# Performance work log

Hardware: AMD Instinct MI355X
Metric: run time of the kernel (lower is better)

## Reference

```python
import jax, jax.numpy as jnp
import numpy as np

N = 8192
TOKEN_DIM = 384
K = 16
D_IN = 2 * (TOKEN_DIM + 3)  # 774


def setup_inputs() -> dict:
    key = jax.random.key(0)
    k1, k2, k3, k4, k5, k6 = jax.random.split(key, 6)
    xyz = jax.random.normal(k1, (N, 3), dtype=jnp.float32)
    feat = jax.random.normal(k2, (N, TOKEN_DIM), dtype=jnp.float32)
    W1 = jax.random.normal(k3, (D_IN, TOKEN_DIM), dtype=jnp.float32) / np.sqrt(D_IN)
    b1 = jax.random.normal(k4, (TOKEN_DIM,), dtype=jnp.float32) * 0.01
    W2 = jax.random.normal(k5, (TOKEN_DIM, 3), dtype=jnp.float32) / np.sqrt(TOKEN_DIM)
    b2 = jax.random.normal(k6, (3,), dtype=jnp.float32) * 0.01
    return {"xyz": xyz, "feat": feat, "W1": W1, "b1": b1, "W2": W2, "b2": b2}


def _knn_idx(xyz, k):
    # pairwise squared distances [N, N]; loop=False -> exclude self via +inf diag
    sq = jnp.sum(xyz * xyz, axis=-1)
    d2 = sq[:, None] + sq[None, :] - 2.0 * (xyz @ xyz.T)
    n = xyz.shape[0]
    d2 = jnp.where(jnp.eye(n, dtype=bool), jnp.inf, d2)
    _, idx = jax.lax.top_k(-d2, k)  # idx[i] = k nearest neighbors (sources) of target i
    return idx


def reference(xyz, feat, W1, b1, W2, b2):
    idx = _knn_idx(xyz, K)                      # [N, K] int32
    x = jnp.concatenate([feat, xyz], axis=-1)   # [N, D] with D = token_dim + 3
    x_j = x[idx]                                # [N, K, D] gathered neighbor feats
    x_i = x[:, None, :]                         # [N, 1, D]
    # EdgeConv message: nn(cat([x_i, x_j - x_i]))
    e = jnp.concatenate([jnp.broadcast_to(x_i, x_j.shape), x_j - x_i], axis=-1)  # [N, K, 2D]
    h = jax.nn.relu(jnp.einsum('nkd,df->nkf', e, W1) + b1)   # [N, K, token_dim]
    m = jnp.einsum('nkf,fo->nko', h, W2) + b2                # [N, K, 3]
    agg = jnp.max(m, axis=1)                                 # max aggregation over neighbors
    return xyz + agg
```

## Files before the change

kernel.cpp:

```cpp
#include <hip/hip_runtime.h>
#include <hip/hip_bf16.h>


#define N 8192
#define TD 384
#define KNN 16
#define DX 387
#define KP 416
#define NF 768
#define INFF __builtin_inff()

typedef __attribute__((ext_vector_type(8))) short short8;
typedef __attribute__((ext_vector_type(4))) float f32x4;
typedef __attribute__((ext_vector_type(2))) float f32x2;


__device__ __forceinline__ f32x2 pk_mul(f32x2 a, f32x2 b) {
    f32x2 r; asm("v_pk_mul_f32 %0, %1, %2" : "=v"(r) : "v"(a), "v"(b)); return r;
}
__device__ __forceinline__ f32x2 pk_add(f32x2 a, f32x2 b) {
    f32x2 r; asm("v_pk_add_f32 %0, %1, %2" : "=v"(r) : "v"(a), "v"(b)); return r;
}
__device__ __forceinline__ f32x2 pk_sub(f32x2 a, f32x2 b) {
    f32x2 r; asm("v_pk_add_f32 %0, %1, %2 neg_lo:[0,1] neg_hi:[0,1]" : "=v"(r) : "v"(a), "v"(b)); return r;
}
__device__ __forceinline__ f32x2 pk_fma(f32x2 a, f32x2 b, f32x2 c) {
    f32x2 r; asm("v_pk_fma_f32 %0, %1, %2, %3" : "=v"(r) : "v"(a), "v"(b), "v"(c)); return r;
}

__device__ __forceinline__ void dist4(f32x2 qx, f32x2 qy, f32x2 qz, f32x2 qw,
                                      f32x2 x01, f32x2 x23, f32x2 y01, f32x2 y23,
                                      f32x2 z01, f32x2 z23, f32x2 s01, f32x2 s23,
                                      f32x2& d01, f32x2& d23) {
    f32x2 dot01 = pk_fma(qz, z01, pk_fma(qy, y01, pk_mul(qx, x01)));
    f32x2 dot23 = pk_fma(qz, z23, pk_fma(qy, y23, pk_mul(qx, x23)));
    d01 = pk_sub(pk_add(qw, s01), pk_add(dot01, dot01));
    d23 = pk_sub(pk_add(qw, s23), pk_add(dot23, dot23));
}

__device__ __forceinline__ int xbin(float x) {
    int b = (int)((x + 4.0f) * 32.0f);
    return b < 0 ? 0 : (b > 255 ? 255 : b);
}


__global__ void __launch_bounds__(128) prep_all(const float* __restrict__ feat,
                                                const float* __restrict__ xyz,
                                                const float* __restrict__ W1,
                                                __hip_bfloat16* __restrict__ Xb,
                                                __hip_bfloat16* __restrict__ Wpt,
                                                int* __restrict__ cut) {
    int b = blockIdx.x;
    int t = threadIdx.x;
    if (b < N) {
        if (t < 96) {
            float4 f = reinterpret_cast<const float4*>(feat + (size_t)b*TD)[t];
            __hip_bfloat16 h[4] = {__float2bfloat16(f.x), __float2bfloat16(f.y),
                                   __float2bfloat16(f.z), __float2bfloat16(f.w)};
            *reinterpret_cast<ulonglong1*>(Xb + b*KP + t*4) = *reinterpret_cast<ulonglong1*>(h);
        } else {
            int d = TD + (t - 96);
            float v = (d < DX) ? xyz[b*3 + (d - TD)] : 0.f;
            Xb[b*KP + d] = __float2bfloat16(v);
        }
    } else if (b < N + NF) {
        int f = b - N;
        for (int k = t; k < KP; k += 128) {
            float v = 0.f;
            if (k < DX) {
                if (f < TD) v = W1[k*TD + f] - W1[(DX+k)*TD + f];
                else        v = W1[(DX+k)*TD + (f - TD)];
            }
            Wpt[f*KP + k] = __float2bfloat16(v);
        }
    } else {
        cut[t] = 0;
        cut[t + 128] = 0;
    }
}


__global__ void __launch_bounds__(256) assign_kernel(const float* __restrict__ xyz,
                                                     int* __restrict__ cut,
                                                     int* __restrict__ tlo,
                                                     int* __restrict__ thi,
                                                     float* __restrict__ stile) {
    __shared__ int hcnt[256];
    __shared__ int base[256];
    __shared__ int stlo[32], sthi[32];
    const int t = threadIdx.x;

    hcnt[t] = 0;
    if (t < 32) { stlo[t] = 255; sthi[t] = 0; }
    __syncthreads();

    #pragma unroll
    for (int c = 0; c < 32; ++c) {
        atomicAdd(&hcnt[xbin(xyz[(t + c*256)*3])], 1);
    }
    __syncthreads();

    const int v = hcnt[t];
    base[t] = v;
    __syncthreads();
    for (int off = 1; off < 256; off <<= 1) {
        int add = (t >= off) ? base[t - off] : 0;
        __syncthreads();
        base[t] += add;
        __syncthreads();
    }
    const int end = base[t], start = end - v;
    __syncthreads();
    base[t] = start;
    __syncthreads();

    if (blockIdx.x == 0) {
        if (v > 0) {
            for (int x = start >> 8; x <= (end - 1) >> 8; ++x) {
                atomicMin(&stlo[x], t);
                atomicMax(&sthi[x], t);
            }
        }
        __syncthreads();
        if (t < 32) { tlo[t] = stlo[t]; thi[t] = sthi[t]; }
    }

    const int i = blockIdx.x * 256 + t;
    float x = xyz[i*3+0], y = xyz[i*3+1], z = xyz[i*3+2];
    int bin = xbin(x);
    int pos = base[bin] + atomicAdd(&cut[bin], 1);
    float sq = __fadd_rn(__fadd_rn(__fmul_rn(x,x), __fmul_rn(y,y)), __fmul_rn(z,z));
    float* tp = stile + (pos >> 8) * 1280 + (pos & 255);
    tp[0] = x; tp[256] = y; tp[512] = z; tp[768] = sq;
    reinterpret_cast<int*>(tp)[1024] = i;
}


__device__ __forceinline__ float rdlane_f(float v, int src) {
    return __uint_as_float(__builtin_amdgcn_readlane(__float_as_uint(v), src));
}
__device__ __forceinline__ unsigned udmap(float x) {
    unsigned u = __float_as_uint(x);
    return ((int)u < 0) ? ~u : (u | 0x80000000u);
}


__global__ void __launch_bounds__(256, 6) knn_kernel(const float* __restrict__ stile,
                                                     const int* __restrict__ tlo,
                                                     const int* __restrict__ thi,
                                                     int* __restrict__ knn) {
    __shared__ float    dcache[4][5][256];
    __shared__ unsigned sbuf[4][128][2];
    const int lane = threadIdx.x & 63;
    const int wv   = threadIdx.x >> 6;
    const int s    = blockIdx.x * 4 + wv;
    const int tq   = s >> 8;
    const int sl   = (s & 255) >> 2;
    const int slot = s & 3;

    const float* qp = stile + tq*1280 + (s & 255);
    const float qx = qp[0], qy = qp[256], qz = qp[512], qw = qp[768];
    const int   qi = reinterpret_cast<const int*>(qp)[1024];
    const f32x2 qx2 = {qx,qx}, qy2 = {qy,qy}, qz2 = {qz,qz}, qw2 = {qw,qw};

    const float* lbase = stile + lane*4;
    const bool is_self_lane = (lane == sl);

    float mn = INFF;
    int lo = tq - 2; if (lo < 0) lo = 0; if (lo > 27) lo = 27;
    #pragma unroll
    for (int tt = 0; tt < 5; ++tt) {
        const int t = lo + tt;
        const float* tp = lbase + t*1280;
        float4 X = *(const float4*)(tp);
        float4 Y = *(const float4*)(tp + 256);
        float4 Z = *(const float4*)(tp + 512);
        float4 S = *(const float4*)(tp + 768);
        f32x2 x01 = {X.x,X.y}, x23 = {X.z,X.w};
        f32x2 y01 = {Y.x,Y.y}, y23 = {Y.z,Y.w};
        f32x2 z01 = {Z.x,Z.y}, z23 = {Z.z,Z.w};
        f32x2 s01 = {S.x,S.y}, s23 = {S.z,S.w};
        f32x2 d01, d23;
        dist4(qx2, qy2, qz2, qw2, x01, x23, y01, y23, z01, z23, s01, s23, d01, d23);
        if ((t == tq) && is_self_lane) {
            if      (slot == 0) d01[0] = INFF;
            else if (slot == 1) d01[1] = INFF;
            else if (slot == 2) d23[0] = INFF;
            else                d23[1] = INFF;
        }
        f32x4 dd = {d01[0], d01[1], d23[0], d23[1]};
        *reinterpret_cast<f32x4*>(&dcache[wv][tt][lane*4]) = dd;
        mn = fminf(mn, fminf(fminf(dd[0], dd[1]), fminf(dd[2], dd[3])));
    }

    float T;
    {
        unsigned ub = udmap(mn);
        unsigned long long alive = ~0ull;
        int need = KNN;
        #pragma unroll
        for (int b = 31; b >= 0; --b) {
            unsigned long long ones  = __ballot(((ub >> b) & 1u) != 0u);
            unsigned long long zeros = alive & ~ones;
            int cz = (int)__popcll(zeros);
            bool tz = (cz >= need);
            alive = tz ? zeros : (alive & ones);
            need  = tz ? need : (need - cz);
        }
        T = fmaxf(rdlane_f(mn, (int)__ffsll(alive) - 1), 0.f);
    }

    unsigned mask;
    {
        const int ti = lane & 31;
        const int bl = tlo[ti], bh = thi[ti];
        const float xlo = (bl == 0)   ? -1e30f : (bl * 0.03125f - 4.0f);
        const float xhi = (bh == 255) ?  1e30f : ((bh + 1) * 0.03125f - 4.0f);
        float gap = fmaxf(0.f, fmaxf(xlo - qx, qx - xhi));
        bool gate = (gap * gap <= T + 1e-3f);
        mask = (unsigned)__ballot(gate && (lane < 32));
    }

    int cnt = 0;
    const unsigned long long ltm = (1ull << lane) - 1;

    auto push = [&](float dv, int idx) {
        bool pred = (dv <= T);
        unsigned long long bal = __ballot(pred);
        if (bal) {
            int posn = cnt + (int)__popcll(bal & ltm);
            if (pred && posn < 128) {
                sbuf[wv][posn][0] = udmap(dv);
                sbuf[wv][posn][1] = (unsigned)idx;
            }
            cnt += (int)__popcll(bal);
        }
    };

    #pragma unroll
    for (int tt = 0; tt < 5; ++tt) {
        const int t = lo + tt;
        if (!((mask >> t) & 1u)) continue;
        f32x4 dd = *reinterpret_cast<const f32x4*>(&dcache[wv][tt][lane*4]);
        int4 I = *(const int4*)(lbase + t*1280 + 1024);
        push(dd[0], I.x);
        push(dd[1], I.y);
        push(dd[2], I.z);
        push(dd[3], I.w);
    }
    unsigned rest = mask & ~(0x1Fu << lo);
    while (rest) {
        const int t = (int)__ffs(rest) - 1;
        rest &= rest - 1;
        const float* tp = lbase + t*1280;
        float4 X = *(const float4*)(tp);
        float4 Y = *(const float4*)(tp + 256);
        float4 Z = *(const float4*)(tp + 512);
        float4 S = *(const float4*)(tp + 768);
        int4   I = *(const int4*)(tp + 1024);
        f32x2 x01 = {X.x,X.y}, x23 = {X.z,X.w};
        f32x2 y01 = {Y.x,Y.y}, y23 = {Y.z,Y.w};
        f32x2 z01 = {Z.x,Z.y}, z23 = {Z.z,Z.w};
        f32x2 s01 = {S.x,S.y}, s23 = {S.z,S.w};
        f32x2 d01, d23;
        dist4(qx2, qy2, qz2, qw2, x01, x23, y01, y23, z01, z23, s01, s23, d01, d23);
        float tmin = fminf(fminf(d01[0], d01[1]), fminf(d23[0], d23[1]));
        if (__ballot(tmin <= T)) {
            push(d01[0], I.x);
            push(d01[1], I.y);
            push(d23[0], I.z);
            push(d23[1], I.w);
        }
    }

    asm volatile("s_waitcnt lgkmcnt(0)" ::: "memory");
    const int M = (cnt > 128) ? 128 : cnt;

    if (M <= 64) {
        unsigned ud1 = 0xFFFFFFFFu, id1 = 0xFFFFFFFFu;
        if (lane < M) { ud1 = sbuf[wv][lane][0]; id1 = sbuf[wv][lane][1]; }
        unsigned long long alive = __ballot(lane < M);
        int need = KNN;
        #pragma unroll
        for (int b = 31; b >= 0; --b) {
            unsigned long long on = __ballot(((ud1 >> b) & 1u) != 0u);
            unsigned long long z  = alive & ~on;
            int cz = (int)__popcll(z);
            bool tz = (cz >= need);
            alive = tz ? z : (alive & on);
            need  = tz ? need : (need - cz);
        }
        unsigned v16 = (unsigned)__builtin_amdgcn_readlane((int)ud1, (int)__ffsll(alive) - 1);
        const bool all_ties = ((int)__popcll(alive) <= need);
        unsigned vidx = 0xFFFFFFFFu;
        if (!all_ties) {
            unsigned long long a = alive;
            int nd = need;
            for (int b = 31; b >= 0; --b) {
                unsigned long long on = __ballot(((id1 >> b) & 1u) != 0u);
                unsigned long long z  = a & ~on;
                int cz = (int)__popcll(z);
                bool tz = (cz >= nd);
                a  = tz ? z : (a & on);
                nd = tz ? nd : (nd - cz);
            }
            vidx = (unsigned)__builtin_amdgcn_readlane((int)id1, (int)__ffsll(a) - 1);
        }
        bool sel = (lane < M) && ((ud1 < v16) || ((ud1 == v16) && (all_ties || (id1 <= vidx))));
        unsigned long long bs = __ballot(sel);
        if (sel) knn[qi*KNN + (int)__popcll(bs & ltm)] = (int)id1;
    } else {
        unsigned ud1 = 0xFFFFFFFFu, id1 = 0xFFFFFFFFu;
        unsigned ud2 = 0xFFFFFFFFu, id2 = 0xFFFFFFFFu;
        if (lane < M)      { ud1 = sbuf[wv][lane][0];      id1 = sbuf[wv][lane][1]; }
        if (lane + 64 < M) { ud2 = sbuf[wv][lane + 64][0]; id2 = sbuf[wv][lane + 64][1]; }

        unsigned long long alive1 = __ballot(lane < M);
        unsigned long long alive2 = __ballot(lane + 64 < M);
        int need = KNN;
        #pragma unroll
        for (int b = 31; b >= 0; --b) {
            unsigned long long on1 = __ballot(((ud1 >> b) & 1u) != 0u);
            unsigned long long on2 = __ballot(((ud2 >> b) & 1u) != 0u);
            unsigned long long z1 = alive1 & ~on1;
            unsigned long long z2 = alive2 & ~on2;
            int cz = (int)__popcll(z1) + (int)__popcll(z2);
            bool tz = (cz >= need);
            alive1 = tz ? z1 : (alive1 & on1);
            alive2 = tz ? z2 : (alive2 & on2);
            need   = tz ? need : (need - cz);
        }
        unsigned v16;
        if (alive1) v16 = (unsigned)__builtin_amdgcn_readlane((int)ud1, (int)__ffsll(alive1) - 1);
        else        v16 = (unsigned)__builtin_amdgcn_readlane((int)ud2, (int)__ffsll(alive2) - 1);

        const int nt = (int)__popcll(alive1) + (int)__popcll(alive2);
        const bool all_ties = (nt <= need);
        unsigned vidx = 0xFFFFFFFFu;
        if (!all_ties) {
            unsigned long long a1 = alive1, a2 = alive2;
            int nd = need;
            for (int b = 31; b >= 0; --b) {
                unsigned long long on1 = __ballot(((id1 >> b) & 1u) != 0u);
                unsigned long long on2 = __ballot(((id2 >> b) & 1u) != 0u);
                unsigned long long z1 = a1 & ~on1;
                unsigned long long z2 = a2 & ~on2;
                int cz = (int)__popcll(z1) + (int)__popcll(z2);
                bool tz = (cz >= nd);
                a1 = tz ? z1 : (a1 & on1);
                a2 = tz ? z2 : (a2 & on2);
                nd = tz ? nd : (nd - cz);
            }
            if (a1) vidx = (unsigned)__builtin_amdgcn_readlane((int)id1, (int)__ffsll(a1) - 1);
            else    vidx = (unsigned)__builtin_amdgcn_readlane((int)id2, (int)__ffsll(a2) - 1);
        }

        bool sel1 = (lane < M)      && ((ud1 < v16) || ((ud1 == v16) && (all_ties || (id1 <= vidx))));
        bool sel2 = (lane + 64 < M) && ((ud2 < v16) || ((ud2 == v16) && (all_ties || (id2 <= vidx))));
        unsigned long long bs1 = __ballot(sel1);
        if (sel1) knn[qi*KNN + (int)__popcll(bs1 & ltm)] = (int)id1;
        const int c1 = (int)__popcll(bs1);
        unsigned long long bs2 = __ballot(sel2);
        if (sel2) knn[qi*KNN + c1 + (int)__popcll(bs2 & ltm)] = (int)id2;
    }
}


__global__ void __launch_bounds__(64) gemm_kernel(const __hip_bfloat16* __restrict__ Xb,
                                                  const __hip_bfloat16* __restrict__ Wpt,
                                                  const float* __restrict__ b1,
                                                  __hip_bfloat16* __restrict__ Ub,
                                                  __hip_bfloat16* __restrict__ Vb) {
    const int lane = threadIdx.x;
    const int i0   = blockIdx.x * 64;
    const int f0   = blockIdx.y * 64;
    const int lm   = lane & 15;
    const int lk   = (lane >> 4) * 8;

    f32x4 acc[4][4];
    #pragma unroll
    for (int r = 0; r < 4; ++r)
        #pragma unroll
        for (int c = 0; c < 4; ++c)
            acc[r][c] = (f32x4){0.f, 0.f, 0.f, 0.f};

    const __hip_bfloat16* xbase = Xb  + (size_t)(i0 + lm) * KP + lk;
    const __hip_bfloat16* wbase = Wpt + (size_t)(f0 + lm) * KP + lk;

    #pragma unroll
    for (int kk = 0; kk < 13; ++kk) {
        short8 a[4], b[4];
        #pragma unroll
        for (int r = 0; r < 4; ++r)
            a[r] = *reinterpret_cast<const short8*>(xbase + (size_t)r*16*KP + kk*32);
        #pragma unroll
        for (int c = 0; c < 4; ++c)
            b[c] = *reinterpret_cast<const short8*>(wbase + (size_t)c*16*KP + kk*32);
        #pragma unroll
        for (int r = 0; r < 4; ++r)
            #pragma unroll
            for (int c = 0; c < 4; ++c)
                acc[r][c] = __builtin_amdgcn_mfma_f32_16x16x32_bf16(a[r], b[c], acc[r][c], 0, 0, 0);
    }

    const bool isU = (f0 < TD);
    __hip_bfloat16* outb = isU ? (Ub + f0) : (Vb + (f0 - TD));
    float bias[4] = {0.f, 0.f, 0.f, 0.f};
    if (isU) {
        #pragma unroll
        for (int c = 0; c < 4; ++c) bias[c] = b1[f0 + c*16 + lm];
    }
    const int crow = (lane >> 4) * 4;
    #pragma unroll
    for (int r = 0; r < 4; ++r)
        #pragma unroll
        for (int c = 0; c < 4; ++c)
            #pragma unroll
            for (int q = 0; q < 4; ++q)
                outb[(size_t)(i0 + r*16 + crow + q) * TD + c*16 + lm] =
                    __float2bfloat16(acc[r][c][q] + bias[c]);
}


__device__ __forceinline__ float bflo(unsigned w) { return __uint_as_float(w << 16); }
__device__ __forceinline__ float bfhi(unsigned w) { return __uint_as_float(w & 0xFFFF0000u); }

template<int CTRL>
__device__ __forceinline__ float dppf(float v) {
    return __uint_as_float((unsigned)__builtin_amdgcn_update_dpp(
        0, (int)__float_as_uint(v), CTRL, 0xF, 0xF, true));
}

__global__ void __launch_bounds__(256) final_kernel(const __hip_bfloat16* __restrict__ Ub,
                                                    const __hip_bfloat16* __restrict__ Vb,
                                                    const int* __restrict__ knn,
                                                    const float* __restrict__ xyz,
                                                    const float* __restrict__ W2,
                                                    const float* __restrict__ b2,
                                                    float* __restrict__ out) {
    const int lane = threadIdx.x & 63;
    const int wv   = threadIdx.x >> 6;
    const int i    = blockIdx.x * 4 + wv;
    const int d0   = lane * 6;

    int jreg = knn[i*KNN + (lane & 15)];

    float u[6], w2l[6][3];
    {
        const unsigned* rowU = reinterpret_cast<const unsigned*>(Ub + (size_t)i * TD) + lane*3;
        unsigned a0 = rowU[0], a1 = rowU[1], a2 = rowU[2];
        u[0] = bflo(a0); u[1] = bfhi(a0);
        u[2] = bflo(a1); u[3] = bfhi(a1);
        u[4] = bflo(a2); u[5] = bfhi(a2);
    }
    #pragma unroll
    for (int t = 0; t < 6; ++t)
        #pragma unroll
        for (int c = 0; c < 3; ++c) w2l[t][c] = W2[(d0 + t)*3 + c];

    const unsigned* vbase = reinterpret_cast<const unsigned*>(Vb);
    const int voff = lane * 3;

    float pk0[16], pk1[16], pk2[16];
    unsigned va[2][4][3];

    #pragma unroll
    for (int t = 0; t < 4; ++t) {
        int j = __builtin_amdgcn_readlane(jreg, t);
        const unsigned* rv = vbase + (size_t)j * 192 + voff;
        va[0][t][0] = rv[0]; va[0][t][1] = rv[1]; va[0][t][2] = rv[2];
    }
    __builtin_amdgcn_sched_barrier(0);

    #pragma unroll
    for (int b = 0; b < 4; ++b) {
        if (b < 3) {
            #pragma unroll
            for (int t = 0; t < 4; ++t) {
                int j = __builtin_amdgcn_readlane(jreg, (b+1)*4 + t);
                const unsigned* rv = vbase + (size_t)j * 192 + voff;
                va[(b+1)&1][t][0] = rv[0];
                va[(b+1)&1][t][1] = rv[1];
                va[(b+1)&1][t][2] = rv[2];
            }
            __builtin_amdgcn_sched_barrier(0);
        }
        #pragma unroll
        for (int t = 0; t < 4; ++t) {
            const int kk = b*4 + t;
            unsigned a0 = va[b&1][t][0], a1 = va[b&1][t][1], a2 = va[b&1][t][2];
            float v0 = bflo(a0), v1 = bfhi(a0);
            float v2 = bflo(a1), v3 = bfhi(a1);
            float v4 = bflo(a2), v5 = bfhi(a2);
            float h0 = fmaxf(u[0] + v0, 0.f), h1 = fmaxf(u[1] + v1, 0.f);
            float h2 = fmaxf(u[2] + v2, 0.f), h3 = fmaxf(u[3] + v3, 0.f);
            float h4 = fmaxf(u[4] + v4, 0.f), h5 = fmaxf(u[5] + v5, 0.f);
            float s0 = 0.f, s1 = 0.f, s2 = 0.f;
            s0 = fmaf(h0, w2l[0][0], s0); s1 = fmaf(h0, w2l[0][1], s1); s2 = fmaf(h0, w2l[0][2], s2);
            s0 = fmaf(h1, w2l[1][0], s0); s1 = fmaf(h1, w2l[1][1], s1); s2 = fmaf(h1, w2l[1][2], s2);
            s0 = fmaf(h2, w2l[2][0], s0); s1 = fmaf(h2, w2l[2][1], s1); s2 = fmaf(h2, w2l[2][2], s2);
            s0 = fmaf(h3, w2l[3][0], s0); s1 = fmaf(h3, w2l[3][1], s1); s2 = fmaf(h3, w2l[3][2], s2);
            s0 = fmaf(h4, w2l[4][0], s0); s1 = fmaf(h4, w2l[4][1], s1); s2 = fmaf(h4, w2l[4][2], s2);
            s0 = fmaf(h5, w2l[5][0], s0); s1 = fmaf(h5, w2l[5][1], s1); s2 = fmaf(h5, w2l[5][2], s2);
            pk0[kk] = s0; pk1[kk] = s1; pk2[kk] = s2;
        }
    }

    #pragma unroll
    for (int kk = 0; kk < 16; ++kk) {
        float r0 = pk0[kk], r1 = pk1[kk], r2 = pk2[kk];
        r0 += dppf<0x121>(r0); r1 += dppf<0x121>(r1); r2 += dppf<0x121>(r2);
        r0 += dppf<0x122>(r0); r1 += dppf<0x122>(r1); r2 += dppf<0x122>(r2);
        r0 += dppf<0x124>(r0); r1 += dppf<0x124>(r1); r2 += dppf<0x124>(r2);
        r0 += dppf<0x128>(r0); r1 += dppf<0x128>(r1); r2 += dppf<0x128>(r2);
        r0 += __shfl_xor(r0, 16); r1 += __shfl_xor(r1, 16); r2 += __shfl_xor(r2, 16);
        r0 += __shfl_xor(r0, 32); r1 += __shfl_xor(r1, 32); r2 += __shfl_xor(r2, 32);
        pk0[kk] = r0; pk1[kk] = r1; pk2[kk] = r2;
    }
    float mx0 = pk0[0], mx1 = pk1[0], mx2 = pk2[0];
    #pragma unroll
    for (int kk = 1; kk < 16; ++kk) {
        mx0 = fmaxf(mx0, pk0[kk]);
        mx1 = fmaxf(mx1, pk1[kk]);
        mx2 = fmaxf(mx2, pk2[kk]);
    }

    if (lane == 0) {
        out[i*3+0] = xyz[i*3+0] + mx0 + b2[0];
        out[i*3+1] = xyz[i*3+1] + mx1 + b2[1];
        out[i*3+2] = xyz[i*3+2] + mx2 + b2[2];
    }
}


extern "C" void kernel_launch(void* const* d_in, const int* in_sizes, int n_in,
                              void* d_out, int out_size, void* d_ws, size_t ws_size,
                              hipStream_t stream) {
    const float* xyz  = (const float*)d_in[0];
    const float* feat = (const float*)d_in[1];
    const float* W1   = (const float*)d_in[2];
    const float* b1   = (const float*)d_in[3];
    const float* W2   = (const float*)d_in[4];
    const float* b2   = (const float*)d_in[5];
    float* out = (float*)d_out;

    char* ws = (char*)d_ws;
    int*            knn   = (int*)(ws + 0);
    float*          stile = (float*)(ws + 524288);
    __hip_bfloat16* Xb    = (__hip_bfloat16*)(ws + 688128);
    __hip_bfloat16* Wpt   = (__hip_bfloat16*)(ws + 7503872);
    __hip_bfloat16* Ub    = (__hip_bfloat16*)(ws + 8142848);
    __hip_bfloat16* Vb    = (__hip_bfloat16*)(ws + 14434304);
    int*            cut   = (int*)(ws + 20725760);
    int*            thi   = (int*)(ws + 20726784);
    int*            tlo   = (int*)(ws + 20726912);

    prep_all     <<<dim3(N + NF + 1),  dim3(128), 0, stream>>>(feat, xyz, W1, Xb, Wpt, cut);
    assign_kernel<<<dim3(N/256),       dim3(256), 0, stream>>>(xyz, cut, tlo, thi, stile);
    knn_kernel   <<<dim3(N/4),         dim3(256), 0, stream>>>(stile, tlo, thi, knn);
    gemm_kernel  <<<dim3(N/64, NF/64), dim3(64),  0, stream>>>(Xb, Wpt, b1, Ub, Vb);
    final_kernel <<<dim3(N/4),         dim3(256), 0, stream>>>(Ub, Vb, knn, xyz, W2, b2, out);
}
```

Baseline: 82.45 us.

## Merge prep with assign and interleave GEMM blocks into the KNN kernel

Folds the prep and binning kernels into one launch. The binning blocks now compute per-block prefix counts locally, which removes the global cut counter and its zeroing. The GEMM is packed as 4 independent waves per 256-thread block and interleaved every sixth block of the KNN launch, so matrix-core work overlaps the VALU-heavy KNN selection. This cuts the launch count from five to three. The radix-select loops also lose full unrolling and gain an early exit once a single candidate remains, trading code size and an extra popcount per iteration for fewer iterations; the KNN kernel also drops its occupancy hint of 6.

```diff
diff --git a/kernel.cpp b/kernel.cpp
--- a/kernel.cpp
+++ b/kernel.cpp
@@ -9,6 +9,11 @@
 #define KP 416
 #define NF 768
 #define INFF __builtin_inff()
+
+#define NB_X (N/2)
+#define NB_W NF
+#define NB_A 32
+#define NGEMM 384
 
 typedef __attribute__((ext_vector_type(8))) short short8;
 typedef __attribute__((ext_vector_type(4))) float f32x4;
@@ -43,29 +48,44 @@
     return b < 0 ? 0 : (b > 255 ? 255 : b);
 }
 
-
-__global__ void __launch_bounds__(128) prep_all(const float* __restrict__ feat,
-                                                const float* __restrict__ xyz,
-                                                const float* __restrict__ W1,
-                                                __hip_bfloat16* __restrict__ Xb,
-                                                __hip_bfloat16* __restrict__ Wpt,
-                                                int* __restrict__ cut) {
-    int b = blockIdx.x;
-    int t = threadIdx.x;
-    if (b < N) {
-        if (t < 96) {
-            float4 f = reinterpret_cast<const float4*>(feat + (size_t)b*TD)[t];
+__device__ __forceinline__ float rdlane_f(float v, int src) {
+    return __uint_as_float(__builtin_amdgcn_readlane(__float_as_uint(v), src));
+}
+__device__ __forceinline__ unsigned udmap(float x) {
+    unsigned u = __float_as_uint(x);
+    return ((int)u < 0) ? ~u : (u | 0x80000000u);
+}
+
+
+__global__ void __launch_bounds__(256) prep_assign(const float* __restrict__ feat,
+                                                   const float* __restrict__ xyz,
+                                                   const float* __restrict__ W1,
+                                                   __hip_bfloat16* __restrict__ Xb,
+                                                   __hip_bfloat16* __restrict__ Wpt,
+                                                   int* __restrict__ tlo,
+                                                   int* __restrict__ thi,
+                                                   float* __restrict__ stile) {
+    const int b = blockIdx.x;
+    const int t = threadIdx.x;
+    if (b < NB_X) {
+        const int half = t >> 7;
+        const int tt = t & 127;
+        const int p = b*2 + half;
+        if (tt < 96) {
+            float4 f = reinterpret_cast<const float4*>(feat + (size_t)p*TD)[tt];
             __hip_bfloat16 h[4] = {__float2bfloat16(f.x), __float2bfloat16(f.y),
                                    __float2bfloat16(f.z), __float2bfloat16(f.w)};
-            *reinterpret_cast<ulonglong1*>(Xb + b*KP + t*4) = *reinterpret_cast<ulonglong1*>(h);
+            *reinterpret_cast<ulonglong1*>(Xb + p*KP + tt*4) = *reinterpret_cast<ulonglong1*>(h);
         } else {
-            int d = TD + (t - 96);
-            float v = (d < DX) ? xyz[b*3 + (d - TD)] : 0.f;
-            Xb[b*KP + d] = __float2bfloat16(v);
-        }
-    } else if (b < N + NF) {
-        int f = b - N;
-        for (int k = t; k < KP; k += 128) {
+            int d = TD + (tt - 96);
+            float v = (d < DX) ? xyz[p*3 + (d - TD)] : 0.f;
+            Xb[p*KP + d] = __float2bfloat16(v);
+        }
+        return;
+    }
+    if (b < NB_X + NB_W) {
+        const int f = b - NB_X;
+        for (int k = t; k < KP; k += 256) {
             float v = 0.f;
             if (k < DX) {
                 if (f < TD) v = W1[k*TD + f] - W1[(DX+k)*TD + f];
@@ -73,62 +93,49 @@
             }
             Wpt[f*KP + k] = __float2bfloat16(v);
         }
-    } else {
-        cut[t] = 0;
-        cut[t + 128] = 0;
-    }
-}
-
-
-__global__ void __launch_bounds__(256) assign_kernel(const float* __restrict__ xyz,
-                                                     int* __restrict__ cut,
-                                                     int* __restrict__ tlo,
-                                                     int* __restrict__ thi,
-                                                     float* __restrict__ stile) {
-    __shared__ int hcnt[256];
-    __shared__ int base[256];
+        return;
+    }
+
+    __shared__ int hcnt[256], pre[256], scan[256], cur[256];
     __shared__ int stlo[32], sthi[32];
-    const int t = threadIdx.x;
-
-    hcnt[t] = 0;
+    const int a = b - (NB_X + NB_W);
+    hcnt[t] = 0; pre[t] = 0; cur[t] = 0;
     if (t < 32) { stlo[t] = 255; sthi[t] = 0; }
     __syncthreads();
 
     #pragma unroll
     for (int c = 0; c < 32; ++c) {
-        atomicAdd(&hcnt[xbin(xyz[(t + c*256)*3])], 1);
+        int bin = xbin(xyz[(c*256 + t)*3]);
+        atomicAdd(&hcnt[bin], 1);
+        if (c < a) atomicAdd(&pre[bin], 1);
     }
     __syncthreads();
 
     const int v = hcnt[t];
-    base[t] = v;
+    scan[t] = v;
     __syncthreads();
     for (int off = 1; off < 256; off <<= 1) {
-        int add = (t >= off) ? base[t - off] : 0;
+        int add = (t >= off) ? scan[t - off] : 0;
         __syncthreads();
-        base[t] += add;
+        scan[t] += add;
         __syncthreads();
     }
-    const int end = base[t], start = end - v;
+    const int end = scan[t], start = end - v;
+    if (a == 0 && v > 0) {
+        for (int x = start >> 8; x <= (end - 1) >> 8; ++x) {
+            atomicMin(&stlo[x], t);
+            atomicMax(&sthi[x], t);
+        }
+    }
     __syncthreads();
-    base[t] = start;
+    scan[t] = start;
     __syncthreads();
-
-    if (blockIdx.x == 0) {
-        if (v > 0) {
-            for (int x = start >> 8; x <= (end - 1) >> 8; ++x) {
-                atomicMin(&stlo[x], t);
-                atomicMax(&sthi[x], t);
-            }
-        }
-        __syncthreads();
-        if (t < 32) { tlo[t] = stlo[t]; thi[t] = sthi[t]; }
-    }
-
-    const int i = blockIdx.x * 256 + t;
+    if (a == 0 && t < 32) { tlo[t] = stlo[t]; thi[t] = sthi[t]; }
+
+    const int i = a*256 + t;
     float x = xyz[i*3+0], y = xyz[i*3+1], z = xyz[i*3+2];
     int bin = xbin(x);
-    int pos = base[bin] + atomicAdd(&cut[bin], 1);
+    int pos = scan[bin] + pre[bin] + atomicAdd(&cur[bin], 1);
     float sq = __fadd_rn(__fadd_rn(__fmul_rn(x,x), __fmul_rn(y,y)), __fmul_rn(z,z));
     float* tp = stile + (pos >> 8) * 1280 + (pos & 255);
     tp[0] = x; tp[256] = y; tp[512] = z; tp[768] = sq;
@@ -136,24 +143,77 @@
 }
 
 
-__device__ __forceinline__ float rdlane_f(float v, int src) {
-    return __uint_as_float(__builtin_amdgcn_readlane(__float_as_uint(v), src));
-}
-__device__ __forceinline__ unsigned udmap(float x) {
-    unsigned u = __float_as_uint(x);
-    return ((int)u < 0) ? ~u : (u | 0x80000000u);
-}
-
-
-__global__ void __launch_bounds__(256, 6) knn_kernel(const float* __restrict__ stile,
-                                                     const int* __restrict__ tlo,
-                                                     const int* __restrict__ thi,
-                                                     int* __restrict__ knn) {
+__global__ void __launch_bounds__(256) knn_gemm(const float* __restrict__ stile,
+                                                const int* __restrict__ tlo,
+                                                const int* __restrict__ thi,
+                                                int* __restrict__ knn,
+                                                const __hip_bfloat16* __restrict__ Xb,
+                                                const __hip_bfloat16* __restrict__ Wpt,
+                                                const float* __restrict__ b1,
+                                                __hip_bfloat16* __restrict__ Ub,
+                                                __hip_bfloat16* __restrict__ Vb) {
     __shared__ float    dcache[4][5][256];
     __shared__ unsigned sbuf[4][128][2];
+    const int u = blockIdx.x;
+    const int g = u / 6;
+    const int r = u - g*6;
     const int lane = threadIdx.x & 63;
     const int wv   = threadIdx.x >> 6;
-    const int s    = blockIdx.x * 4 + wv;
+
+    if ((r == 5) && (g < NGEMM)) {
+        const int tid = g*4 + wv;
+        const int i0  = (tid & 127) * 64;
+        const int f0  = (tid >> 7) * 64;
+        const int lm  = lane & 15;
+        const int lk  = (lane >> 4) * 8;
+
+        f32x4 acc[4][4];
+        #pragma unroll
+        for (int rr = 0; rr < 4; ++rr)
+            #pragma unroll
+            for (int c = 0; c < 4; ++c)
+                acc[rr][c] = (f32x4){0.f, 0.f, 0.f, 0.f};
+
+        const __hip_bfloat16* xbase = Xb  + (size_t)(i0 + lm) * KP + lk;
+        const __hip_bfloat16* wbase = Wpt + (size_t)(f0 + lm) * KP + lk;
+
+        #pragma unroll
+        for (int kk = 0; kk < 13; ++kk) {
+            short8 aa[4], bb[4];
+            #pragma unroll
+            for (int rr = 0; rr < 4; ++rr)
+                aa[rr] = *reinterpret_cast<const short8*>(xbase + (size_t)rr*16*KP + kk*32);
+            #pragma unroll
+            for (int c = 0; c < 4; ++c)
+                bb[c] = *reinterpret_cast<const short8*>(wbase + (size_t)c*16*KP + kk*32);
+            #pragma unroll
+            for (int rr = 0; rr < 4; ++rr)
+                #pragma unroll
+                for (int c = 0; c < 4; ++c)
+                    acc[rr][c] = __builtin_amdgcn_mfma_f32_16x16x32_bf16(aa[rr], bb[c], acc[rr][c], 0, 0, 0);
+        }
+
+        const bool isU = (f0 < TD);
+        __hip_bfloat16* outb = isU ? (Ub + f0) : (Vb + (f0 - TD));
+        float bias[4] = {0.f, 0.f, 0.f, 0.f};
+        if (isU) {
+            #pragma unroll
+            for (int c = 0; c < 4; ++c) bias[c] = b1[f0 + c*16 + lm];
+        }
+        const int crow = (lane >> 4) * 4;
+        #pragma unroll
+        for (int rr = 0; rr < 4; ++rr)
+            #pragma unroll
+            for (int c = 0; c < 4; ++c)
+                #pragma unroll
+                for (int q = 0; q < 4; ++q)
+                    outb[(size_t)(i0 + rr*16 + crow + q) * TD + c*16 + lm] =
+                        __float2bfloat16(acc[rr][c][q] + bias[c]);
+        return;
+    }
+
+    const int kb = u - ((g < NGEMM) ? g : NGEMM);
+    const int s  = kb * 4 + wv;
     const int tq   = s >> 8;
     const int sl   = (s & 255) >> 2;
     const int slot = s & 3;
@@ -198,8 +258,8 @@
         unsigned ub = udmap(mn);
         unsigned long long alive = ~0ull;
         int need = KNN;
-        #pragma unroll
         for (int b = 31; b >= 0; --b) {
+            if (__popcll(alive) == 1) break;
             unsigned long long ones  = __ballot(((ub >> b) & 1u) != 0u);
             unsigned long long zeros = alive & ~ones;
             int cz = (int)__popcll(zeros);
@@ -281,8 +341,8 @@
         if (lane < M) { ud1 = sbuf[wv][lane][0]; id1 = sbuf[wv][lane][1]; }
         unsigned long long alive = __ballot(lane < M);
         int need = KNN;
-        #pragma unroll
         for (int b = 31; b >= 0; --b) {
+            if (__popcll(alive) == 1) break;
             unsigned long long on = __ballot(((ud1 >> b) & 1u) != 0u);
             unsigned long long z  = alive & ~on;
             int cz = (int)__popcll(z);
@@ -297,6 +357,7 @@
             unsigned long long a = alive;
             int nd = need;
             for (int b = 31; b >= 0; --b) {
+                if (__popcll(a) == 1) break;
                 unsigned long long on = __ballot(((id1 >> b) & 1u) != 0u);
                 unsigned long long z  = a & ~on;
                 int cz = (int)__popcll(z);
@@ -318,8 +379,8 @@
         unsigned long long alive1 = __ballot(lane < M);
         unsigned long long alive2 = __ballot(lane + 64 < M);
         int need = KNN;
-        #pragma unroll
         for (int b = 31; b >= 0; --b) {
+            if ((int)__popcll(alive1) + (int)__popcll(alive2) == 1) break;
             unsigned long long on1 = __ballot(((ud1 >> b) & 1u) != 0u);
             unsigned long long on2 = __ballot(((ud2 >> b) & 1u) != 0u);
             unsigned long long z1 = alive1 & ~on1;
@@ -341,6 +402,7 @@
             unsigned long long a1 = alive1, a2 = alive2;
             int nd = need;
             for (int b = 31; b >= 0; --b) {
+                if ((int)__popcll(a1) + (int)__popcll(a2) == 1) break;
                 unsigned long long on1 = __ballot(((id1 >> b) & 1u) != 0u);
                 unsigned long long on2 = __ballot(((id2 >> b) & 1u) != 0u);
                 unsigned long long z1 = a1 & ~on1;
@@ -363,62 +425,6 @@
         unsigned long long bs2 = __ballot(sel2);
         if (sel2) knn[qi*KNN + c1 + (int)__popcll(bs2 & ltm)] = (int)id2;
     }
-}
-
-
-__global__ void __launch_bounds__(64) gemm_kernel(const __hip_bfloat16* __restrict__ Xb,
-                                                  const __hip_bfloat16* __restrict__ Wpt,
-                                                  const float* __restrict__ b1,
-                                                  __hip_bfloat16* __restrict__ Ub,
-                                                  __hip_bfloat16* __restrict__ Vb) {
-    const int lane = threadIdx.x;
-    const int i0   = blockIdx.x * 64;
-    const int f0   = blockIdx.y * 64;
-    const int lm   = lane & 15;
-    const int lk   = (lane >> 4) * 8;
-
-    f32x4 acc[4][4];
-    #pragma unroll
-    for (int r = 0; r < 4; ++r)
-        #pragma unroll
-        for (int c = 0; c < 4; ++c)
-            acc[r][c] = (f32x4){0.f, 0.f, 0.f, 0.f};
-
-    const __hip_bfloat16* xbase = Xb  + (size_t)(i0 + lm) * KP + lk;
-    const __hip_bfloat16* wbase = Wpt + (size_t)(f0 + lm) * KP + lk;
-
-    #pragma unroll
-    for (int kk = 0; kk < 13; ++kk) {
-        short8 a[4], b[4];
-        #pragma unroll
-        for (int r = 0; r < 4; ++r)
-            a[r] = *reinterpret_cast<const short8*>(xbase + (size_t)r*16*KP + kk*32);
-        #pragma unroll
-        for (int c = 0; c < 4; ++c)
-            b[c] = *reinterpret_cast<const short8*>(wbase + (size_t)c*16*KP + kk*32);
-        #pragma unroll
-        for (int r = 0; r < 4; ++r)
-            #pragma unroll
-            for (int c = 0; c < 4; ++c)
-                acc[r][c] = __builtin_amdgcn_mfma_f32_16x16x32_bf16(a[r], b[c], acc[r][c], 0, 0, 0);
-    }
-
-    const bool isU = (f0 < TD);
-    __hip_bfloat16* outb = isU ? (Ub + f0) : (Vb + (f0 - TD));
-    float bias[4] = {0.f, 0.f, 0.f, 0.f};
-    if (isU) {
-        #pragma unroll
-        for (int c = 0; c < 4; ++c) bias[c] = b1[f0 + c*16 + lm];
-    }
-    const int crow = (lane >> 4) * 4;
-    #pragma unroll
-    for (int r = 0; r < 4; ++r)
-        #pragma unroll
-        for (int c = 0; c < 4; ++c)
-            #pragma unroll
-            for (int q = 0; q < 4; ++q)
-                outb[(size_t)(i0 + r*16 + crow + q) * TD + c*16 + lm] =
-                    __float2bfloat16(acc[r][c][q] + bias[c]);
 }
 
 
@@ -551,13 +557,13 @@
     __hip_bfloat16* Wpt   = (__hip_bfloat16*)(ws + 7503872);
     __hip_bfloat16* Ub    = (__hip_bfloat16*)(ws + 8142848);
     __hip_bfloat16* Vb    = (__hip_bfloat16*)(ws + 14434304);
-    int*            cut   = (int*)(ws + 20725760);
-    int*            thi   = (int*)(ws + 20726784);
-    int*            tlo   = (int*)(ws + 20726912);
-
-    prep_all     <<<dim3(N + NF + 1),  dim3(128), 0, stream>>>(feat, xyz, W1, Xb, Wpt, cut);
-    assign_kernel<<<dim3(N/256),       dim3(256), 0, stream>>>(xyz, cut, tlo, thi, stile);
-    knn_kernel   <<<dim3(N/4),         dim3(256), 0, stream>>>(stile, tlo, thi, knn);
-    gemm_kernel  <<<dim3(N/64, NF/64), dim3(64),  0, stream>>>(Xb, Wpt, b1, Ub, Vb);
-    final_kernel <<<dim3(N/4),         dim3(256), 0, stream>>>(Ub, Vb, knn, xyz, W2, b2, out);
-}
+    int*            thi   = (int*)(ws + 20725760);
+    int*            tlo   = (int*)(ws + 20725888);
+
+    prep_assign <<<dim3(NB_X + NB_W + NB_A),       dim3(256), 0, stream>>>(
+        feat, xyz, W1, Xb, Wpt, tlo, thi, stile);
+    knn_gemm    <<<dim3(N/4 + NGEMM),              dim3(256), 0, stream>>>(
+        stile, tlo, thi, knn, Xb, Wpt, b1, Ub, Vb);
+    final_kernel<<<dim3(N/4),                      dim3(256), 0, stream>>>(
+        Ub, Vb, knn, xyz, W2, b2, out);
+}
```

Result: no change. 82.55 us (+0.1%).
